# Performance work log

Measured on AMD Instinct MI355X. Metric: run time of the kernel, lower is better.

## Reference

```python
import jax, jax.numpy as jnp
import numpy as np

N_NODES = 100000
D_FEAT = 128
N_EDGES = 1600000
N_ROWS = 50000  # batch of target nodes


def setup_inputs() -> dict:
    key = jax.random.key(0)
    k1, k2, k3 = jax.random.split(key, 3)
    features = jax.random.normal(k1, (N_NODES, D_FEAT), dtype=jnp.float32)
    neigh_ids = jax.random.randint(k2, (N_EDGES,), 0, N_NODES, dtype=jnp.int64)
    row_ids = jnp.sort(jax.random.randint(k3, (N_EDGES,), 0, N_ROWS, dtype=jnp.int64))
    return {
        "features": features,
        "neigh_ids": neigh_ids,
        "row_ids": row_ids,
        "num_segments": N_ROWS,
    }


def reference(features, neigh_ids, row_ids, num_segments):
    # Gather neighbor embeddings: [E, D]
    gathered = features[neigh_ids]
    # Per-row sum and count -> mean (matches mask.mm with values 1/deg)
    sums = jax.ops.segment_sum(gathered, row_ids, num_segments=num_segments)
    counts = jax.ops.segment_sum(
        jnp.ones((neigh_ids.shape[0],), dtype=features.dtype),
        row_ids,
        num_segments=num_segments,
    )
    to_feats = sums / jnp.maximum(counts, 1.0)[:, None]
    return to_feats
```

## Files before the change

### kernel.cpp

```cpp
#include <hip/hip_runtime.h>

#define D_FEAT 128
#define WAVE 64

__device__ __forceinline__ unsigned short f32_to_bf16_rn(float f) {
    unsigned int u = __float_as_uint(f);
    unsigned int r = u + 0x7fffu + ((u >> 16) & 1u);
    return (unsigned short)(r >> 16);
}

__global__ void build_row_start(const int* __restrict__ rids,
                                int* __restrict__ row_start,
                                int n_edges, int n_rows) {
    int e = blockIdx.x * blockDim.x + threadIdx.x;
    if (e >= n_edges) return;
    int r_cur  = rids[e];
    int r_prev = (e == 0) ? -1 : rids[e - 1];
    for (int r = r_prev + 1; r <= r_cur; ++r) row_start[r] = e;
    if (e == n_edges - 1) {
        for (int r = r_cur + 1; r <= n_rows; ++r) row_start[r] = n_edges;
    }
}

__global__ void convert_bf16(const float* __restrict__ feats,
                             unsigned short* __restrict__ tbl,
                             int n_elems, int total) {
    int i = (blockIdx.x * blockDim.x + threadIdx.x) * 4;
    if (i >= total) return;
    if (i + 4 <= n_elems) {
        float4 v = *(const float4*)(feats + i);
        ushort4 o;
        o.x = f32_to_bf16_rn(v.x);
        o.y = f32_to_bf16_rn(v.y);
        o.z = f32_to_bf16_rn(v.z);
        o.w = f32_to_bf16_rn(v.w);
        *(ushort4*)(tbl + i) = o;
    } else {
        for (int k = 0; k < 4 && i + k < total; ++k)
            tbl[i + k] = (i + k < n_elems) ? f32_to_bf16_rn(feats[i + k])
                                           : (unsigned short)0;
    }
}

__global__ void mean_agg_kernel(const unsigned short* __restrict__ tbl,
                                const int* __restrict__ nids,
                                const int* __restrict__ row_start,
                                float* __restrict__ out,
                                int n_rows, int zero_row) {
    int wave = (blockIdx.x * blockDim.x + threadIdx.x) / WAVE;
    int lane = threadIdx.x & (WAVE - 1);
    if (wave >= n_rows) return;

    const int q   = lane >> 4;
    const int sub = lane & 15;

    int lo = row_start[wave];
    int hi = row_start[wave + 1];

    float acc[8];
    #pragma unroll
    for (int k = 0; k < 8; ++k) acc[k] = 0.f;

    int e = lo;
    for (; e + 32 <= hi; e += 32) {
        uint4 u[8];
        #pragma unroll
        for (int g = 0; g < 8; ++g) {
            int nid = nids[e + 4 * g + q];
            u[g] = *(const uint4*)(tbl + (size_t)nid * D_FEAT + sub * 8);
        }
        #pragma unroll
        for (int g = 0; g < 8; ++g) {
            acc[0] += __uint_as_float(u[g].x << 16);
            acc[1] += __uint_as_float(u[g].x & 0xffff0000u);
            acc[2] += __uint_as_float(u[g].y << 16);
            acc[3] += __uint_as_float(u[g].y & 0xffff0000u);
            acc[4] += __uint_as_float(u[g].z << 16);
            acc[5] += __uint_as_float(u[g].z & 0xffff0000u);
            acc[6] += __uint_as_float(u[g].w << 16);
            acc[7] += __uint_as_float(u[g].w & 0xffff0000u);
        }
    }
    #pragma unroll
    for (int g = 0; g < 8; ++g) {
        int base = e + 4 * g;
        if (base < hi) {
            int idx = base + q;
            int nid = (idx < hi) ? nids[idx] : zero_row;
            uint4 u = *(const uint4*)(tbl + (size_t)nid * D_FEAT + sub * 8);
            acc[0] += __uint_as_float(u.x << 16);
            acc[1] += __uint_as_float(u.x & 0xffff0000u);
            acc[2] += __uint_as_float(u.y << 16);
            acc[3] += __uint_as_float(u.y & 0xffff0000u);
            acc[4] += __uint_as_float(u.z << 16);
            acc[5] += __uint_as_float(u.z & 0xffff0000u);
            acc[6] += __uint_as_float(u.w << 16);
            acc[7] += __uint_as_float(u.w & 0xffff0000u);
        }
    }

    #pragma unroll
    for (int k = 0; k < 8; ++k) {
        acc[k] += __shfl_xor(acc[k], 16, WAVE);
        acc[k] += __shfl_xor(acc[k], 32, WAVE);
    }

    int deg = hi - lo;
    float inv = 1.0f / (float)(deg > 0 ? deg : 1);
    if (q == 0) {
        float* dst = out + (size_t)wave * D_FEAT + sub * 8;
        float4 o0 = make_float4(acc[0] * inv, acc[1] * inv, acc[2] * inv, acc[3] * inv);
        float4 o1 = make_float4(acc[4] * inv, acc[5] * inv, acc[6] * inv, acc[7] * inv);
        *(float4*)dst = o0;
        *(float4*)(dst + 4) = o1;
    }
}

extern "C" void kernel_launch(void* const* d_in, const int* in_sizes, int n_in,
                              void* d_out, int out_size, void* d_ws, size_t ws_size,
                              hipStream_t stream) {
    const float* feats = (const float*)d_in[0];
    const int* nids    = (const int*)d_in[1];
    const int* rids    = (const int*)d_in[2];
    float* out         = (float*)d_out;

    int n_feat_elems = in_sizes[0];
    int n_nodes      = n_feat_elems / D_FEAT;
    int n_edges      = in_sizes[1];
    int n_rows       = out_size / D_FEAT;

    unsigned short* tbl = (unsigned short*)d_ws;
    size_t tbl_bytes = (size_t)(n_nodes + 1) * D_FEAT * sizeof(unsigned short);
    tbl_bytes = (tbl_bytes + 255) & ~(size_t)255;
    int* row_start = (int*)((char*)d_ws + tbl_bytes);

    const int BLOCK = 256;

    int total_tbl = (n_nodes + 1) * D_FEAT;
    int grid_c = (total_tbl / 4 + BLOCK - 1) / BLOCK;
    convert_bf16<<<grid_c, BLOCK, 0, stream>>>(feats, tbl, n_feat_elems, total_tbl);

    int grid_b = (n_edges + BLOCK - 1) / BLOCK;
    build_row_start<<<grid_b, BLOCK, 0, stream>>>(rids, row_start, n_edges, n_rows);

    int waves_per_block = BLOCK / WAVE;
    int grid_a = (n_rows + waves_per_block - 1) / waves_per_block;
    mean_agg_kernel<<<grid_a, BLOCK, 0, stream>>>(tbl, nids, row_start, out,
                                                  n_rows, n_nodes);
}
```

Measured before the change: 170.5 us.

## Widen bf16 conversion stores and simplify gather loop into single masked 16-edge pass

The conversion kernel now handles 8 floats per thread and writes one 16-byte store instead of an 8-byte one. The aggregation loop drops the 32-edge unrolled body and its separate tail, using one loop of 16 edges per iteration with clamped index loads. The feature table is addressed as uint4 with 32-bit offsets, and launch bounds are added. The output write is split across two quarter-waves, each writing one float4. Fewer loads stay in flight per iteration, which may reduce latency hiding in the gather, in exchange for lower register pressure and simpler control flow.

```diff
diff --git a/kernel.cpp b/kernel.cpp
--- a/kernel.cpp
+++ b/kernel.cpp
@@ -25,29 +25,31 @@
 __global__ void convert_bf16(const float* __restrict__ feats,
                              unsigned short* __restrict__ tbl,
                              int n_elems, int total) {
-    int i = (blockIdx.x * blockDim.x + threadIdx.x) * 4;
+    int i = (blockIdx.x * blockDim.x + threadIdx.x) * 8;
     if (i >= total) return;
-    if (i + 4 <= n_elems) {
-        float4 v = *(const float4*)(feats + i);
-        ushort4 o;
-        o.x = f32_to_bf16_rn(v.x);
-        o.y = f32_to_bf16_rn(v.y);
-        o.z = f32_to_bf16_rn(v.z);
-        o.w = f32_to_bf16_rn(v.w);
-        *(ushort4*)(tbl + i) = o;
+    if (i + 8 <= n_elems) {
+        float4 a = *(const float4*)(feats + i);
+        float4 b = *(const float4*)(feats + i + 4);
+        uint4 o;
+        o.x = (unsigned)f32_to_bf16_rn(a.x) | ((unsigned)f32_to_bf16_rn(a.y) << 16);
+        o.y = (unsigned)f32_to_bf16_rn(a.z) | ((unsigned)f32_to_bf16_rn(a.w) << 16);
+        o.z = (unsigned)f32_to_bf16_rn(b.x) | ((unsigned)f32_to_bf16_rn(b.y) << 16);
+        o.w = (unsigned)f32_to_bf16_rn(b.z) | ((unsigned)f32_to_bf16_rn(b.w) << 16);
+        *(uint4*)(tbl + i) = o;
     } else {
-        for (int k = 0; k < 4 && i + k < total; ++k)
+        for (int k = 0; k < 8 && i + k < total; ++k)
             tbl[i + k] = (i + k < n_elems) ? f32_to_bf16_rn(feats[i + k])
                                            : (unsigned short)0;
     }
 }
 
-__global__ void mean_agg_kernel(const unsigned short* __restrict__ tbl,
-                                const int* __restrict__ nids,
-                                const int* __restrict__ row_start,
-                                float* __restrict__ out,
-                                int n_rows, int zero_row) {
-    int wave = (blockIdx.x * blockDim.x + threadIdx.x) / WAVE;
+__global__ void __launch_bounds__(256)
+mean_agg_kernel(const uint4* __restrict__ tbl4,
+                const int* __restrict__ nids,
+                const int* __restrict__ row_start,
+                float* __restrict__ out,
+                int n_rows, int zero_row) {
+    int wave = (blockIdx.x * blockDim.x + threadIdx.x) >> 6;
     int lane = threadIdx.x & (WAVE - 1);
     if (wave >= n_rows) return;
 
@@ -61,33 +63,15 @@
     #pragma unroll
     for (int k = 0; k < 8; ++k) acc[k] = 0.f;
 
-    int e = lo;
-    for (; e + 32 <= hi; e += 32) {
-        uint4 u[8];
+    for (int e = lo; e < hi; e += 16) {
         #pragma unroll
-        for (int g = 0; g < 8; ++g) {
-            int nid = nids[e + 4 * g + q];
-            u[g] = *(const uint4*)(tbl + (size_t)nid * D_FEAT + sub * 8);
-        }
-        #pragma unroll
-        for (int g = 0; g < 8; ++g) {
-            acc[0] += __uint_as_float(u[g].x << 16);
-            acc[1] += __uint_as_float(u[g].x & 0xffff0000u);
-            acc[2] += __uint_as_float(u[g].y << 16);
-            acc[3] += __uint_as_float(u[g].y & 0xffff0000u);
-            acc[4] += __uint_as_float(u[g].z << 16);
-            acc[5] += __uint_as_float(u[g].z & 0xffff0000u);
-            acc[6] += __uint_as_float(u[g].w << 16);
-            acc[7] += __uint_as_float(u[g].w & 0xffff0000u);
-        }
-    }
-    #pragma unroll
-    for (int g = 0; g < 8; ++g) {
-        int base = e + 4 * g;
-        if (base < hi) {
-            int idx = base + q;
-            int nid = (idx < hi) ? nids[idx] : zero_row;
-            uint4 u = *(const uint4*)(tbl + (size_t)nid * D_FEAT + sub * 8);
+        for (int g = 0; g < 4; ++g) {
+            int idx = e + 4 * g + q;
+            int idc = idx < hi ? idx : hi - 1;
+            int nid = nids[idc];
+            nid = idx < hi ? nid : zero_row;
+            unsigned off = ((unsigned)nid << 4) + (unsigned)sub;
+            uint4 u = tbl4[off];
             acc[0] += __uint_as_float(u.x << 16);
             acc[1] += __uint_as_float(u.x & 0xffff0000u);
             acc[2] += __uint_as_float(u.y << 16);
@@ -107,12 +91,14 @@
 
     int deg = hi - lo;
     float inv = 1.0f / (float)(deg > 0 ? deg : 1);
-    if (q == 0) {
-        float* dst = out + (size_t)wave * D_FEAT + sub * 8;
-        float4 o0 = make_float4(acc[0] * inv, acc[1] * inv, acc[2] * inv, acc[3] * inv);
-        float4 o1 = make_float4(acc[4] * inv, acc[5] * inv, acc[6] * inv, acc[7] * inv);
-        *(float4*)dst = o0;
-        *(float4*)(dst + 4) = o1;
+
+    if (q < 2) {
+        float4 o;
+        o.x = (q == 0 ? acc[0] : acc[4]) * inv;
+        o.y = (q == 0 ? acc[1] : acc[5]) * inv;
+        o.z = (q == 0 ? acc[2] : acc[6]) * inv;
+        o.w = (q == 0 ? acc[3] : acc[7]) * inv;
+        *(float4*)(out + (size_t)wave * D_FEAT + sub * 8 + q * 4) = o;
     }
 }
 
@@ -137,7 +123,7 @@
     const int BLOCK = 256;
 
     int total_tbl = (n_nodes + 1) * D_FEAT;
-    int grid_c = (total_tbl / 4 + BLOCK - 1) / BLOCK;
+    int grid_c = ((total_tbl + 7) / 8 + BLOCK - 1) / BLOCK;
     convert_bf16<<<grid_c, BLOCK, 0, stream>>>(feats, tbl, n_feat_elems, total_tbl);
 
     int grid_b = (n_edges + BLOCK - 1) / BLOCK;
@@ -145,6 +131,6 @@
 
     int waves_per_block = BLOCK / WAVE;
     int grid_a = (n_rows + waves_per_block - 1) / waves_per_block;
-    mean_agg_kernel<<<grid_a, BLOCK, 0, stream>>>(tbl, nids, row_start, out,
-                                                  n_rows, n_nodes);
+    mean_agg_kernel<<<grid_a, BLOCK, 0, stream>>>((const uint4*)tbl, nids, row_start,
+                                                  out, n_rows, n_nodes);
 }
```

After: 156.3 us. 8.3% less time.
